# Optimization experiments

Measured on AMD Instinct MI355X. Metric: run time of the kernel, lower is better.

Reference implementation:

```python
import jax, jax.numpy as jnp
import numpy as np

N, E = 100000, 1600000
C_IN, C_HID, C_OUT = 64, 128, 64
EPS_MSG = 1e-7   # GENConv message eps
EPS_BN = 1e-5    # BatchNorm eps


def setup_inputs() -> dict:
    key = jax.random.key(0)
    ks = jax.random.split(key, 8)
    glorot = lambda k, shp, fan: jax.random.normal(k, shp, jnp.float32) * (1.0 / np.sqrt(fan))
    return dict(
        x=jax.random.normal(ks[0], (N, C_IN), jnp.float32),
        edge_index=jax.random.randint(ks[1], (2, E), 0, N, jnp.int32),
        edge_attr=jax.random.normal(ks[2], (E, C_IN), jnp.float32),
        pos=jax.random.normal(ks[3], (N, 3), jnp.float32),
        # GENConv internal MLP: Linear -> BN -> ReLU -> Linear
        W1=glorot(ks[4], (C_IN, C_HID), C_IN), b1=jnp.zeros((C_HID,), jnp.float32),
        g_mlp=jnp.ones((C_HID,), jnp.float32), be_mlp=jnp.zeros((C_HID,), jnp.float32),
        W2=glorot(ks[5], (C_HID, C_OUT), C_HID), b2=jnp.zeros((C_OUT,), jnp.float32),
        # block: BN -> SiLU -> Linear(no bias) -> BN -> SiLU
        g1=jnp.ones((C_OUT,), jnp.float32), be1=jnp.zeros((C_OUT,), jnp.float32),
        Wl=glorot(ks[6], (C_OUT, C_OUT), C_OUT),
        g2=jnp.ones((C_OUT,), jnp.float32), be2=jnp.zeros((C_OUT,), jnp.float32),
    )


def _bn(h, g, b):
    # training-mode batch norm over the node dimension
    m = h.mean(0)
    v = jnp.mean((h - m) ** 2, axis=0)
    return (h - m) * jax.lax.rsqrt(v + EPS_BN) * g + b


def reference(x, edge_index, edge_attr, pos, W1, b1, g_mlp, be_mlp, W2, b2,
              g1, be1, Wl, g2, be2):
    src, dst = edge_index[0], edge_index[1]
    # GENConv message: relu(x_j + e_attr) + eps, shape [E, C_IN]
    msg = jax.nn.relu(x[src] + edge_attr) + EPS_MSG
    # softmax aggregation over incoming edges per destination node (t = 1)
    mx = jax.ops.segment_max(msg, dst, num_segments=N)
    mx = jnp.where(jnp.isfinite(mx), mx, 0.0)  # guard empty segments
    ex = jnp.exp(msg - mx[dst])
    den = jax.ops.segment_sum(ex, dst, num_segments=N)
    w = ex / (den[dst] + 1e-16)
    aggr = jax.ops.segment_sum(msg * w, dst, num_segments=N)  # [N, C_IN]
    # root add + internal MLP (Linear -> BN -> ReLU -> Linear)
    h = aggr + x
    h = jax.nn.relu(_bn(h @ W1 + b1, g_mlp, be_mlp)) @ W2 + b2
    # block tail: BN -> SiLU -> Linear(no bias) -> BN -> SiLU
    h = jax.nn.silu(_bn(h, g1, be1))
    h = jax.nn.silu(_bn(h @ Wl, g2, be2))
    return h
```

## Files before the change

### kernel.cpp

```cpp
#include <hip/hip_runtime.h>

#define N_NODES 100000
#define E_EDGES 1600000
#define CIN 64
#define CHID 128
#define COUT 64
#define NT 64
#define NB ((N_NODES + NT - 1) / NT)
#define RBLK 64
#define CAP 128

__global__ void bucket_kernel(const int* __restrict__ ei, int* __restrict__ cnt,
                              int2* __restrict__ es) {
    int e = blockIdx.x * blockDim.x + threadIdx.x;
    if (e < E_EDGES) {
        int src = ei[e];
        int dst = ei[E_EDGES + e];
        int p = atomicAdd(&cnt[dst], 1);
        if (p < CAP) es[((long)dst << 7) + p] = make_int2(e, src);
    }
}

__global__ void gather_kernel(const float* __restrict__ x,
                              const float* __restrict__ ea,
                              const int2* __restrict__ es,
                              const int* __restrict__ cnt,
                              float* __restrict__ h0) {
    int node = (blockIdx.x * blockDim.x + threadIdx.x) >> 6;
    int lane = threadIdx.x & 63;
    if (node >= N_NODES) return;
    long s = (long)node << 7;
    int n = cnt[node];
    n = n > CAP ? CAP : n;
    float nm = 0.f, dn = 0.f;
    int p = 0;
    for (; p + 16 <= n; p += 16) {
        int2 q[16];
#pragma unroll
        for (int u = 0; u < 16; ++u) q[u] = es[s + p + u];
        float av[16], xv[16];
#pragma unroll
        for (int u = 0; u < 16; ++u)
            av[u] = __builtin_nontemporal_load(ea + (long)q[u].x * CIN + lane);
#pragma unroll
        for (int u = 0; u < 16; ++u) xv[u] = x[(long)q[u].y * CIN + lane];
#pragma unroll
        for (int u = 0; u < 16; ++u) {
            float m = fmaxf(xv[u] + av[u], 0.f) + 1e-7f;
            float ex = __expf(m);
            nm = fmaf(m, ex, nm);
            dn += ex;
        }
    }
    for (; p + 8 <= n; p += 8) {
        int2 q[8];
#pragma unroll
        for (int u = 0; u < 8; ++u) q[u] = es[s + p + u];
        float av[8], xv[8];
#pragma unroll
        for (int u = 0; u < 8; ++u)
            av[u] = __builtin_nontemporal_load(ea + (long)q[u].x * CIN + lane);
#pragma unroll
        for (int u = 0; u < 8; ++u) xv[u] = x[(long)q[u].y * CIN + lane];
#pragma unroll
        for (int u = 0; u < 8; ++u) {
            float m = fmaxf(xv[u] + av[u], 0.f) + 1e-7f;
            float ex = __expf(m);
            nm = fmaf(m, ex, nm);
            dn += ex;
        }
    }
    for (; p + 4 <= n; p += 4) {
        int2 q[4];
#pragma unroll
        for (int u = 0; u < 4; ++u) q[u] = es[s + p + u];
        float av[4], xv[4];
#pragma unroll
        for (int u = 0; u < 4; ++u)
            av[u] = __builtin_nontemporal_load(ea + (long)q[u].x * CIN + lane);
#pragma unroll
        for (int u = 0; u < 4; ++u) xv[u] = x[(long)q[u].y * CIN + lane];
#pragma unroll
        for (int u = 0; u < 4; ++u) {
            float m = fmaxf(xv[u] + av[u], 0.f) + 1e-7f;
            float ex = __expf(m);
            nm = fmaf(m, ex, nm);
            dn += ex;
        }
    }
    for (; p < n; ++p) {
        int2 q = es[s + p];
        float m = fmaxf(x[(long)q.y * CIN + lane] + ea[(long)q.x * CIN + lane], 0.f) + 1e-7f;
        float ex = __expf(m);
        nm = fmaf(m, ex, nm);
        dn += ex;
    }
    h0[(long)node * CIN + lane] = nm / (dn + 1e-16f) + x[(long)node * CIN + lane];
}

__global__ void reduce_slab_kernel(const float* __restrict__ P, int totrows,
                                   int rows_per, float* __restrict__ Q,
                                   float* __restrict__ mr, int C, float invN,
                                   int* __restrict__ ticket) {
    int C2 = blockDim.x;
    int t = threadIdx.x;
    long r0 = (long)blockIdx.x * rows_per;
    long r1 = r0 + rows_per;
    if (r1 > totrows) r1 = totrows;
    {
        float s0 = 0.f, s1 = 0.f, s2 = 0.f, s3 = 0.f;
        long r = r0;
        for (; r + 4 <= r1; r += 4) {
            s0 += P[(r + 0) * C2 + t];
            s1 += P[(r + 1) * C2 + t];
            s2 += P[(r + 2) * C2 + t];
            s3 += P[(r + 3) * C2 + t];
        }
        for (; r < r1; ++r) s0 += P[r * C2 + t];
        Q[(long)blockIdx.x * C2 + t] = (s0 + s1) + (s2 + s3);
    }
    __threadfence();
    __shared__ int lastFlag;
    if (t == 0) lastFlag = (atomicAdd(ticket, 1) == (int)gridDim.x - 1);
    __syncthreads();
    if (!lastFlag) return;
    __threadfence();
    float s0 = 0.f, s1 = 0.f, s2 = 0.f, s3 = 0.f;
    for (int r = 0; r < RBLK; r += 4) {
        s0 += Q[(long)(r + 0) * C2 + t];
        s1 += Q[(long)(r + 1) * C2 + t];
        s2 += Q[(long)(r + 2) * C2 + t];
        s3 += Q[(long)(r + 3) * C2 + t];
    }
    __shared__ float sm[256];
    sm[t] = (s0 + s1) + (s2 + s3);
    __syncthreads();
    if (t < C) {
        float m = sm[t] * invN;
        float v = sm[C + t] * invN - m * m;
        mr[t] = m;
        mr[C + t] = rsqrtf(fmaxf(v, 0.f) + 1e-5f);
    }
}

__global__ void __launch_bounds__(256) gemm1_kernel(
        const float* __restrict__ h0, const float* __restrict__ W1,
        const float* __restrict__ b1, float* __restrict__ t1,
        float* __restrict__ P) {
    __shared__ float sW[CIN * CHID];
    __shared__ float sh[NT * CIN];
    int tid = threadIdx.x;
    int nbase = blockIdx.x * NT;
    for (int i = tid * 4; i < CIN * CHID; i += 1024)
        *(float4*)&sW[i] = *(const float4*)&W1[i];
    for (int i = tid * 4; i < NT * CIN; i += 1024) {
        int node = nbase + (i >> 6);
        float4 v = make_float4(0.f, 0.f, 0.f, 0.f);
        if (node < N_NODES) v = *(const float4*)&h0[(long)node * CIN + (i & 63)];
        *(float4*)&sh[i] = v;
    }
    __syncthreads();
    int js = (tid & 31) * 4;
    int r  = tid >> 5;
    float4 bb = *(const float4*)&b1[js];
    float acc[8][4];
#pragma unroll
    for (int i = 0; i < 8; ++i) { acc[i][0]=bb.x; acc[i][1]=bb.y; acc[i][2]=bb.z; acc[i][3]=bb.w; }
#pragma unroll 4
    for (int k = 0; k < CIN; ++k) {
        float4 w = *(float4*)&sW[k * CHID + js];
#pragma unroll
        for (int i = 0; i < 8; ++i) {
            float a = sh[(r * 8 + i) * CIN + k];
            acc[i][0] = fmaf(a, w.x, acc[i][0]);
            acc[i][1] = fmaf(a, w.y, acc[i][1]);
            acc[i][2] = fmaf(a, w.z, acc[i][2]);
            acc[i][3] = fmaf(a, w.w, acc[i][3]);
        }
    }
    float s1[4] = {0,0,0,0}, s2[4] = {0,0,0,0};
#pragma unroll
    for (int i = 0; i < 8; ++i) {
        int node = nbase + r * 8 + i;
        if (node < N_NODES) {
            *(float4*)&t1[(long)node * CHID + js] =
                make_float4(acc[i][0], acc[i][1], acc[i][2], acc[i][3]);
#pragma unroll
            for (int jj = 0; jj < 4; ++jj) {
                s1[jj] += acc[i][jj];
                s2[jj] += acc[i][jj] * acc[i][jj];
            }
        }
    }
    __syncthreads();
    float* red = sW;
    *(float4*)&red[r * 128 + js]        = make_float4(s1[0], s1[1], s1[2], s1[3]);
    *(float4*)&red[1024 + r * 128 + js] = make_float4(s2[0], s2[1], s2[2], s2[3]);
    __syncthreads();
    {
        int base = (tid < 128) ? tid : (1024 + tid - 128);
        float v = 0.f;
#pragma unroll
        for (int rr = 0; rr < 8; ++rr) v += red[base + rr * 128];
        P[(long)blockIdx.x * 256 + tid] = v;
    }
}

__global__ void __launch_bounds__(256) gemm2_kernel(
        const float* __restrict__ t1, const float* __restrict__ mr1,
        const float* __restrict__ g, const float* __restrict__ be,
        const float* __restrict__ W2, const float* __restrict__ b2,
        float* __restrict__ h2, float* __restrict__ P) {
    __shared__ float sW[CHID * COUT];
    __shared__ float sr[NT * CHID];
    int tid = threadIdx.x;
    int nbase = blockIdx.x * NT;
    for (int i = tid * 4; i < CHID * COUT; i += 1024)
        *(float4*)&sW[i] = *(const float4*)&W2[i];
    for (int i = tid * 4; i < NT * CHID; i += 1024) {
        int node = nbase + (i >> 7);
        int j = i & 127;
        float4 v = make_float4(0.f, 0.f, 0.f, 0.f);
        if (node < N_NODES) {
            v = *(const float4*)&t1[(long)node * CHID + j];
            float4 mn = *(const float4*)&mr1[j];
            float4 rq = *(const float4*)&mr1[CHID + j];
            float4 gg = *(const float4*)&g[j];
            float4 bb = *(const float4*)&be[j];
            v.x = fmaxf((v.x - mn.x) * rq.x * gg.x + bb.x, 0.f);
            v.y = fmaxf((v.y - mn.y) * rq.y * gg.y + bb.y, 0.f);
            v.z = fmaxf((v.z - mn.z) * rq.z * gg.z + bb.z, 0.f);
            v.w = fmaxf((v.w - mn.w) * rq.w * gg.w + bb.w, 0.f);
        }
        *(float4*)&sr[i] = v;
    }
    __syncthreads();
    int js = (tid & 15) * 4;
    int r  = tid >> 4;
    float4 bb = *(const float4*)&b2[js];
    float acc[4][4];
#pragma unroll
    for (int i = 0; i < 4; ++i) { acc[i][0]=bb.x; acc[i][1]=bb.y; acc[i][2]=bb.z; acc[i][3]=bb.w; }
#pragma unroll 4
    for (int k = 0; k < CHID; ++k) {
        float4 w = *(float4*)&sW[k * COUT + js];
#pragma unroll
        for (int i = 0; i < 4; ++i) {
            float a = sr[(r * 4 + i) * CHID + k];
            acc[i][0] = fmaf(a, w.x, acc[i][0]);
            acc[i][1] = fmaf(a, w.y, acc[i][1]);
            acc[i][2] = fmaf(a, w.z, acc[i][2]);
            acc[i][3] = fmaf(a, w.w, acc[i][3]);
        }
    }
    float s1[4] = {0,0,0,0}, s2[4] = {0,0,0,0};
#pragma unroll
    for (int i = 0; i < 4; ++i) {
        int node = nbase + r * 4 + i;
        if (node < N_NODES) {
            *(float4*)&h2[(long)node * COUT + js] =
                make_float4(acc[i][0], acc[i][1], acc[i][2], acc[i][3]);
#pragma unroll
            for (int jj = 0; jj < 4; ++jj) {
                s1[jj] += acc[i][jj];
                s2[jj] += acc[i][jj] * acc[i][jj];
            }
        }
    }
    __syncthreads();
    float* red = sW;
    *(float4*)&red[r * 64 + js]        = make_float4(s1[0], s1[1], s1[2], s1[3]);
    *(float4*)&red[1024 + r * 64 + js] = make_float4(s2[0], s2[1], s2[2], s2[3]);
    __syncthreads();
    if (tid < 128) {
        int base = (tid < 64) ? tid : (1024 + tid - 64);
        float v = 0.f;
#pragma unroll
        for (int rr = 0; rr < 16; ++rr) v += red[base + rr * 64];
        P[(long)blockIdx.x * 128 + tid] = v;
    }
}

__global__ void __launch_bounds__(256) gemm3_kernel(
        const float* __restrict__ h2, const float* __restrict__ mr2,
        const float* __restrict__ g, const float* __restrict__ be,
        const float* __restrict__ Wl,
        float* __restrict__ t3, float* __restrict__ P) {
    __shared__ float sW[COUT * COUT];
    __shared__ float sr[NT * COUT];
    int tid = threadIdx.x;
    int nbase = blockIdx.x * NT;
    for (int i = tid * 4; i < COUT * COUT; i += 1024)
        *(float4*)&sW[i] = *(const float4*)&Wl[i];
    for (int i = tid * 4; i < NT * COUT; i += 1024) {
        int node = nbase + (i >> 6);
        int j = i & 63;
        float4 v = make_float4(0.f, 0.f, 0.f, 0.f);
        if (node < N_NODES) {
            v = *(const float4*)&h2[(long)node * COUT + j];
            float4 mn = *(const float4*)&mr2[j];
            float4 rq = *(const float4*)&mr2[COUT + j];
            float4 gg = *(const float4*)&g[j];
            float4 bb = *(const float4*)&be[j];
            v.x = (v.x - mn.x) * rq.x * gg.x + bb.x;
            v.y = (v.y - mn.y) * rq.y * gg.y + bb.y;
            v.z = (v.z - mn.z) * rq.z * gg.z + bb.z;
            v.w = (v.w - mn.w) * rq.w * gg.w + bb.w;
            v.x = v.x / (1.f + __expf(-v.x));
            v.y = v.y / (1.f + __expf(-v.y));
            v.z = v.z / (1.f + __expf(-v.z));
            v.w = v.w / (1.f + __expf(-v.w));
        }
        *(float4*)&sr[i] = v;
    }
    __syncthreads();
    int js = (tid & 15) * 4;
    int r  = tid >> 4;
    float acc[4][4];
#pragma unroll
    for (int i = 0; i < 4; ++i) { acc[i][0]=0.f; acc[i][1]=0.f; acc[i][2]=0.f; acc[i][3]=0.f; }
#pragma unroll 4
    for (int k = 0; k < COUT; ++k) {
        float4 w = *(float4*)&sW[k * COUT + js];
#pragma unroll
        for (int i = 0; i < 4; ++i) {
            float a = sr[(r * 4 + i) * COUT + k];
            acc[i][0] = fmaf(a, w.x, acc[i][0]);
            acc[i][1] = fmaf(a, w.y, acc[i][1]);
            acc[i][2] = fmaf(a, w.z, acc[i][2]);
            acc[i][3] = fmaf(a, w.w, acc[i][3]);
        }
    }
    float s1[4] = {0,0,0,0}, s2[4] = {0,0,0,0};
#pragma unroll
    for (int i = 0; i < 4; ++i) {
        int node = nbase + r * 4 + i;
        if (node < N_NODES) {
            *(float4*)&t3[(long)node * COUT + js] =
                make_float4(acc[i][0], acc[i][1], acc[i][2], acc[i][3]);
#pragma unroll
            for (int jj = 0; jj < 4; ++jj) {
                s1[jj] += acc[i][jj];
                s2[jj] += acc[i][jj] * acc[i][jj];
            }
        }
    }
    __syncthreads();
    float* red = sW;
    *(float4*)&red[r * 64 + js]        = make_float4(s1[0], s1[1], s1[2], s1[3]);
    *(float4*)&red[1024 + r * 64 + js] = make_float4(s2[0], s2[1], s2[2], s2[3]);
    __syncthreads();
    if (tid < 128) {
        int base = (tid < 64) ? tid : (1024 + tid - 64);
        float v = 0.f;
#pragma unroll
        for (int rr = 0; rr < 16; ++rr) v += red[base + rr * 64];
        P[(long)blockIdx.x * 128 + tid] = v;
    }
}

__global__ void final_kernel(const float* __restrict__ t3, const float* __restrict__ mr3,
                             const float* __restrict__ g, const float* __restrict__ be,
                             float* __restrict__ out) {
    long i = ((long)blockIdx.x * blockDim.x + threadIdx.x) * 4;
    int j = (int)(i & 63);
    float4 v = *(const float4*)&t3[i];
    float4 mn = *(const float4*)&mr3[j];
    float4 rq = *(const float4*)&mr3[COUT + j];
    float4 gg = *(const float4*)&g[j];
    float4 bb = *(const float4*)&be[j];
    v.x = (v.x - mn.x) * rq.x * gg.x + bb.x;
    v.y = (v.y - mn.y) * rq.y * gg.y + bb.y;
    v.z = (v.z - mn.z) * rq.z * gg.z + bb.z;
    v.w = (v.w - mn.w) * rq.w * gg.w + bb.w;
    v.x = v.x / (1.f + __expf(-v.x));
    v.y = v.y / (1.f + __expf(-v.y));
    v.z = v.z / (1.f + __expf(-v.z));
    v.w = v.w / (1.f + __expf(-v.w));
    *(float4*)&out[i] = v;
}

extern "C" void kernel_launch(void* const* d_in, const int* in_sizes, int n_in,
                              void* d_out, int out_size, void* d_ws, size_t ws_size,
                              hipStream_t stream) {
    const float* x   = (const float*)d_in[0];
    const int*   ei  = (const int*)d_in[1];
    const float* ea  = (const float*)d_in[2];
    const float* W1  = (const float*)d_in[4];
    const float* b1  = (const float*)d_in[5];
    const float* gm  = (const float*)d_in[6];
    const float* bm  = (const float*)d_in[7];
    const float* W2  = (const float*)d_in[8];
    const float* b2  = (const float*)d_in[9];
    const float* g1  = (const float*)d_in[10];
    const float* be1 = (const float*)d_in[11];
    const float* Wl  = (const float*)d_in[12];
    const float* g2  = (const float*)d_in[13];
    const float* be2 = (const float*)d_in[14];
    float* out = (float*)d_out;

    float* h0   = (float*)d_ws;
    float* t1   = h0 + (long)N_NODES * CIN;
    float* h2   = t1 + (long)N_NODES * CHID;
    float* t3   = h0;
    float* Sfin = h2 + (long)N_NODES * COUT;
    float* Q    = Sfin + 512;
    int*   cnt  = (int*)(Q + RBLK * 256);
    int*   tickets = cnt + N_NODES;
    long   es_off = ((long)(N_NODES * CIN) + (long)N_NODES * CHID + (long)N_NODES * COUT
                     + 512 + RBLK * 256 + N_NODES + 4 + 255) & ~255L;
    int2*  es   = (int2*)((float*)d_ws + es_off);
    float* P1 = h2;
    float* P2 = h0;
    float* P3 = t1;

    const float invN = 1.f / N_NODES;

    hipMemsetAsync(cnt, 0, ((size_t)N_NODES + 4) * sizeof(int), stream);

    bucket_kernel<<<(E_EDGES + 255) / 256, 256, 0, stream>>>(ei, cnt, es);
    gather_kernel<<<(N_NODES * 64 + 255) / 256, 256, 0, stream>>>(x, ea, es, cnt, h0);

    const int rpA = (NB + RBLK - 1) / RBLK;

    gemm1_kernel<<<NB, 256, 0, stream>>>(h0, W1, b1, t1, P1);
    reduce_slab_kernel<<<RBLK, 256, 0, stream>>>(P1, NB, rpA, Q, Sfin, CHID, invN, tickets + 0);
    gemm2_kernel<<<NB, 256, 0, stream>>>(t1, Sfin, gm, bm, W2, b2, h2, P2);
    reduce_slab_kernel<<<RBLK, 128, 0, stream>>>(P2, NB, rpA, Q, Sfin + 256, COUT, invN, tickets + 1);
    gemm3_kernel<<<NB, 256, 0, stream>>>(h2, Sfin + 256, g1, be1, Wl, t3, P3);
    reduce_slab_kernel<<<RBLK, 128, 0, stream>>>(P3, NB, rpA, Q, Sfin + 384, COUT, invN, tickets + 2);
    final_kernel<<<(N_NODES * COUT / 4) / 256, 256, 0, stream>>>(t3, Sfin + 384, g2, be2, out);
}
```

Measured before the change: 371.7 us.

## Compute first BN stats from input second moments and fuse GEMM1 with GEMM2

The first batch-norm statistics are now derived algebraically from the mean and 64x64 second-moment matrix of h0 combined with W1, so the 128-wide hidden activation no longer has to be written out first. GEMM1 and GEMM2 are fused into one kernel that keeps the hidden tile in LDS, which removes the t1 write and re-read and one launch. Bias b1 is dropped because the batch norm cancels it. The trade-offs are an extra moment pass over h0, 80KB of LDS per block (which lowers occupancy), and possible cancellation error in the E[x²]-mean² variance formula.

Result: slower. 449.7 us (+21.0%).

```diff
diff --git a/kernel.cpp b/kernel.cpp
--- a/kernel.cpp
+++ b/kernel.cpp
@@ -9,6 +9,9 @@
 #define NB ((N_NODES + NT - 1) / NT)
 #define RBLK 64
 #define CAP 128
+#define SBLK 256
+#define SROWS ((N_NODES + SBLK - 1) / SBLK)
+#define SPSTRIDE 4160
 
 __global__ void bucket_kernel(const int* __restrict__ ei, int* __restrict__ cnt,
                               int2* __restrict__ es) {
@@ -96,6 +99,197 @@
         dn += ex;
     }
     h0[(long)node * CIN + lane] = nm / (dn + 1e-16f) + x[(long)node * CIN + lane];
+}
+
+__global__ void __launch_bounds__(256) smom_kernel(const float* __restrict__ h0,
+                                                   float* __restrict__ Sp) {
+    __shared__ float sh[64 * 64];
+    int tid = threadIdx.x;
+    int i4 = (tid & 15) * 4;
+    int j4 = (tid >> 4) * 4;
+    float acc[4][4];
+#pragma unroll
+    for (int a = 0; a < 4; ++a) { acc[a][0]=0.f; acc[a][1]=0.f; acc[a][2]=0.f; acc[a][3]=0.f; }
+    float msum = 0.f;
+    int n0 = blockIdx.x * SROWS;
+    int n1 = n0 + SROWS;
+    if (n1 > N_NODES) n1 = N_NODES;
+    for (int t0 = n0; t0 < n1; t0 += 64) {
+        int tn = n1 - t0; if (tn > 64) tn = 64;
+        __syncthreads();
+        for (int idx = tid * 4; idx < 64 * 64; idx += 1024) {
+            int nl = idx >> 6;
+            float4 v = make_float4(0.f, 0.f, 0.f, 0.f);
+            if (nl < tn) v = *(const float4*)&h0[(long)(t0 + nl) * CIN + (idx & 63)];
+            *(float4*)&sh[idx] = v;
+        }
+        __syncthreads();
+#pragma unroll 2
+        for (int nl = 0; nl < tn; ++nl) {
+            float hi[4], hj[4];
+#pragma unroll
+            for (int a = 0; a < 4; ++a) hi[a] = sh[nl * 64 + i4 + a];
+#pragma unroll
+            for (int b = 0; b < 4; ++b) hj[b] = sh[nl * 64 + j4 + b];
+#pragma unroll
+            for (int a = 0; a < 4; ++a)
+#pragma unroll
+                for (int b = 0; b < 4; ++b) acc[a][b] = fmaf(hi[a], hj[b], acc[a][b]);
+            if (tid < 64) msum += sh[nl * 64 + tid];
+        }
+    }
+    float* p = Sp + (long)blockIdx.x * SPSTRIDE;
+#pragma unroll
+    for (int a = 0; a < 4; ++a)
+        *(float4*)&p[(i4 + a) * 64 + j4] = make_float4(acc[a][0], acc[a][1], acc[a][2], acc[a][3]);
+    if (tid < 64) p[4096 + tid] = msum;
+}
+
+__global__ void __launch_bounds__(256) sred_kernel(const float* __restrict__ Sp,
+        const float* __restrict__ W1, float* __restrict__ Sfull,
+        float* __restrict__ mr1, float invN, int* __restrict__ ticket) {
+    int tid = threadIdx.x;
+    int idx = blockIdx.x * 256 + tid;
+    float s = 0.f;
+    for (int p = 0; p < SBLK; ++p) s += Sp[(long)p * SPSTRIDE + idx];
+    Sfull[idx] = s;
+    if (blockIdx.x == 0 && tid < 64) {
+        float m = 0.f;
+        for (int p = 0; p < SBLK; ++p) m += Sp[(long)p * SPSTRIDE + 4096 + tid];
+        Sfull[4096 + tid] = m;
+    }
+    __threadfence();
+    __shared__ int lastFlag;
+    if (tid == 0) lastFlag = (atomicAdd(ticket, 1) == (int)gridDim.x - 1);
+    __syncthreads();
+    if (!lastFlag) return;
+    __threadfence();
+    __shared__ float sS[4096 + 64];
+    __shared__ float sW[CIN * CHID];
+    __shared__ float redQ[256], redM[256];
+    for (int k = tid; k < 4096 + 64; k += 256) sS[k] = Sfull[k];
+    for (int k = tid; k < CIN * CHID; k += 256) sW[k] = W1[k];
+    __syncthreads();
+    int j = tid & 127;
+    int half = tid >> 7;
+    float q = 0.f, ml = 0.f;
+    for (int i = half * 32; i < half * 32 + 32; ++i) {
+        float wi = sW[i * CHID + j];
+        float inner = 0.f;
+#pragma unroll 4
+        for (int k = 0; k < 64; ++k) inner = fmaf(sS[i * 64 + k], sW[k * CHID + j], inner);
+        q = fmaf(wi, inner, q);
+        ml = fmaf(sS[4096 + i], wi, ml);
+    }
+    redQ[tid] = q; redM[tid] = ml;
+    __syncthreads();
+    if (tid < 128) {
+        float qf = redQ[tid] + redQ[tid + 128];
+        float mlf = (redM[tid] + redM[tid + 128]) * invN;
+        float var = qf * invN - mlf * mlf;
+        mr1[tid] = mlf;
+        mr1[128 + tid] = rsqrtf(fmaxf(var, 0.f) + 1e-5f);
+    }
+}
+
+__global__ void __launch_bounds__(256) gemm12_kernel(
+        const float* __restrict__ h0, const float* __restrict__ W1,
+        const float* __restrict__ mr1, const float* __restrict__ g1v,
+        const float* __restrict__ be1v,
+        const float* __restrict__ W2, const float* __restrict__ b2,
+        float* __restrict__ h2, float* __restrict__ P) {
+    __shared__ float lds[20480];
+    float* sW1 = lds;
+    float* sW2 = lds + 8192;
+    float* sh  = lds + 16384;
+    int tid = threadIdx.x;
+    int nbase = blockIdx.x * NT;
+    for (int i = tid * 4; i < 8192; i += 1024) *(float4*)&sW1[i] = *(const float4*)&W1[i];
+    for (int i = tid * 4; i < 8192; i += 1024) *(float4*)&sW2[i] = *(const float4*)&W2[i];
+    for (int i = tid * 4; i < 4096; i += 1024) {
+        int node = nbase + (i >> 6);
+        float4 v = make_float4(0.f, 0.f, 0.f, 0.f);
+        if (node < N_NODES) v = *(const float4*)&h0[(long)node * CIN + (i & 63)];
+        *(float4*)&sh[i] = v;
+    }
+    __syncthreads();
+    int js = (tid & 31) * 4;
+    int r  = tid >> 5;
+    float acc[8][4];
+#pragma unroll
+    for (int i = 0; i < 8; ++i) { acc[i][0]=0.f; acc[i][1]=0.f; acc[i][2]=0.f; acc[i][3]=0.f; }
+#pragma unroll 4
+    for (int k = 0; k < CIN; ++k) {
+        float4 w = *(float4*)&sW1[k * CHID + js];
+#pragma unroll
+        for (int i = 0; i < 8; ++i) {
+            float a = sh[(r * 8 + i) * CIN + k];
+            acc[i][0] = fmaf(a, w.x, acc[i][0]);
+            acc[i][1] = fmaf(a, w.y, acc[i][1]);
+            acc[i][2] = fmaf(a, w.z, acc[i][2]);
+            acc[i][3] = fmaf(a, w.w, acc[i][3]);
+        }
+    }
+    float4 mn = *(const float4*)&mr1[js];
+    float4 rs = *(const float4*)&mr1[128 + js];
+    float4 gg = *(const float4*)&g1v[js];
+    float4 bb = *(const float4*)&be1v[js];
+    __syncthreads();
+    float* sr = lds;
+#pragma unroll
+    for (int i = 0; i < 8; ++i) {
+        float4 v;
+        v.x = fmaxf((acc[i][0] - mn.x) * rs.x * gg.x + bb.x, 0.f);
+        v.y = fmaxf((acc[i][1] - mn.y) * rs.y * gg.y + bb.y, 0.f);
+        v.z = fmaxf((acc[i][2] - mn.z) * rs.z * gg.z + bb.z, 0.f);
+        v.w = fmaxf((acc[i][3] - mn.w) * rs.w * gg.w + bb.w, 0.f);
+        *(float4*)&sr[(r * 8 + i) * CHID + js] = v;
+    }
+    __syncthreads();
+    int js2 = (tid & 15) * 4;
+    int r2  = tid >> 4;
+    float4 b2v = *(const float4*)&b2[js2];
+    float acc2[4][4];
+#pragma unroll
+    for (int i = 0; i < 4; ++i) { acc2[i][0]=b2v.x; acc2[i][1]=b2v.y; acc2[i][2]=b2v.z; acc2[i][3]=b2v.w; }
+#pragma unroll 4
+    for (int k = 0; k < CHID; ++k) {
+        float4 w = *(float4*)&sW2[k * COUT + js2];
+#pragma unroll
+        for (int i = 0; i < 4; ++i) {
+            float a = sr[(r2 * 4 + i) * CHID + k];
+            acc2[i][0] = fmaf(a, w.x, acc2[i][0]);
+            acc2[i][1] = fmaf(a, w.y, acc2[i][1]);
+            acc2[i][2] = fmaf(a, w.z, acc2[i][2]);
+            acc2[i][3] = fmaf(a, w.w, acc2[i][3]);
+        }
+    }
+    float s1[4] = {0,0,0,0}, s2[4] = {0,0,0,0};
+#pragma unroll
+    for (int i = 0; i < 4; ++i) {
+        int node = nbase + r2 * 4 + i;
+        if (node < N_NODES) {
+            *(float4*)&h2[(long)node * COUT + js2] =
+                make_float4(acc2[i][0], acc2[i][1], acc2[i][2], acc2[i][3]);
+#pragma unroll
+            for (int jj = 0; jj < 4; ++jj) {
+                s1[jj] += acc2[i][jj];
+                s2[jj] += acc2[i][jj] * acc2[i][jj];
+            }
+        }
+    }
+    __syncthreads();
+    float* red = lds + 16384;
+    *(float4*)&red[r2 * 64 + js2]        = make_float4(s1[0], s1[1], s1[2], s1[3]);
+    *(float4*)&red[1024 + r2 * 64 + js2] = make_float4(s2[0], s2[1], s2[2], s2[3]);
+    __syncthreads();
+    if (tid < 128) {
+        int base = (tid < 64) ? tid : (1024 + tid - 64);
+        float v = 0.f;
+#pragma unroll
+        for (int rr = 0; rr < 16; ++rr) v += red[base + rr * 64];
+        P[(long)blockIdx.x * 128 + tid] = v;
+    }
 }
 
 __global__ void reduce_slab_kernel(const float* __restrict__ P, int totrows,
@@ -140,144 +334,6 @@
         float v = sm[C + t] * invN - m * m;
         mr[t] = m;
         mr[C + t] = rsqrtf(fmaxf(v, 0.f) + 1e-5f);
-    }
-}
-
-__global__ void __launch_bounds__(256) gemm1_kernel(
-        const float* __restrict__ h0, const float* __restrict__ W1,
-        const float* __restrict__ b1, float* __restrict__ t1,
-        float* __restrict__ P) {
-    __shared__ float sW[CIN * CHID];
-    __shared__ float sh[NT * CIN];
-    int tid = threadIdx.x;
-    int nbase = blockIdx.x * NT;
-    for (int i = tid * 4; i < CIN * CHID; i += 1024)
-        *(float4*)&sW[i] = *(const float4*)&W1[i];
-    for (int i = tid * 4; i < NT * CIN; i += 1024) {
-        int node = nbase + (i >> 6);
-        float4 v = make_float4(0.f, 0.f, 0.f, 0.f);
-        if (node < N_NODES) v = *(const float4*)&h0[(long)node * CIN + (i & 63)];
-        *(float4*)&sh[i] = v;
-    }
-    __syncthreads();
-    int js = (tid & 31) * 4;
-    int r  = tid >> 5;
-    float4 bb = *(const float4*)&b1[js];
-    float acc[8][4];
-#pragma unroll
-    for (int i = 0; i < 8; ++i) { acc[i][0]=bb.x; acc[i][1]=bb.y; acc[i][2]=bb.z; acc[i][3]=bb.w; }
-#pragma unroll 4
-    for (int k = 0; k < CIN; ++k) {
-        float4 w = *(float4*)&sW[k * CHID + js];
-#pragma unroll
-        for (int i = 0; i < 8; ++i) {
-            float a = sh[(r * 8 + i) * CIN + k];
-            acc[i][0] = fmaf(a, w.x, acc[i][0]);
-            acc[i][1] = fmaf(a, w.y, acc[i][1]);
-            acc[i][2] = fmaf(a, w.z, acc[i][2]);
-            acc[i][3] = fmaf(a, w.w, acc[i][3]);
-        }
-    }
-    float s1[4] = {0,0,0,0}, s2[4] = {0,0,0,0};
-#pragma unroll
-    for (int i = 0; i < 8; ++i) {
-        int node = nbase + r * 8 + i;
-        if (node < N_NODES) {
-            *(float4*)&t1[(long)node * CHID + js] =
-                make_float4(acc[i][0], acc[i][1], acc[i][2], acc[i][3]);
-#pragma unroll
-            for (int jj = 0; jj < 4; ++jj) {
-                s1[jj] += acc[i][jj];
-                s2[jj] += acc[i][jj] * acc[i][jj];
-            }
-        }
-    }
-    __syncthreads();
-    float* red = sW;
-    *(float4*)&red[r * 128 + js]        = make_float4(s1[0], s1[1], s1[2], s1[3]);
-    *(float4*)&red[1024 + r * 128 + js] = make_float4(s2[0], s2[1], s2[2], s2[3]);
-    __syncthreads();
-    {
-        int base = (tid < 128) ? tid : (1024 + tid - 128);
-        float v = 0.f;
-#pragma unroll
-        for (int rr = 0; rr < 8; ++rr) v += red[base + rr * 128];
-        P[(long)blockIdx.x * 256 + tid] = v;
-    }
-}
-
-__global__ void __launch_bounds__(256) gemm2_kernel(
-        const float* __restrict__ t1, const float* __restrict__ mr1,
-        const float* __restrict__ g, const float* __restrict__ be,
-        const float* __restrict__ W2, const float* __restrict__ b2,
-        float* __restrict__ h2, float* __restrict__ P) {
-    __shared__ float sW[CHID * COUT];
-    __shared__ float sr[NT * CHID];
-    int tid = threadIdx.x;
-    int nbase = blockIdx.x * NT;
-    for (int i = tid * 4; i < CHID * COUT; i += 1024)
-        *(float4*)&sW[i] = *(const float4*)&W2[i];
-    for (int i = tid * 4; i < NT * CHID; i += 1024) {
-        int node = nbase + (i >> 7);
-        int j = i & 127;
-        float4 v = make_float4(0.f, 0.f, 0.f, 0.f);
-        if (node < N_NODES) {
-            v = *(const float4*)&t1[(long)node * CHID + j];
-            float4 mn = *(const float4*)&mr1[j];
-            float4 rq = *(const float4*)&mr1[CHID + j];
-            float4 gg = *(const float4*)&g[j];
-            float4 bb = *(const float4*)&be[j];
-            v.x = fmaxf((v.x - mn.x) * rq.x * gg.x + bb.x, 0.f);
-            v.y = fmaxf((v.y - mn.y) * rq.y * gg.y + bb.y, 0.f);
-            v.z = fmaxf((v.z - mn.z) * rq.z * gg.z + bb.z, 0.f);
-            v.w = fmaxf((v.w - mn.w) * rq.w * gg.w + bb.w, 0.f);
-        }
-        *(float4*)&sr[i] = v;
-    }
-    __syncthreads();
-    int js = (tid & 15) * 4;
-    int r  = tid >> 4;
-    float4 bb = *(const float4*)&b2[js];
-    float acc[4][4];
-#pragma unroll
-    for (int i = 0; i < 4; ++i) { acc[i][0]=bb.x; acc[i][1]=bb.y; acc[i][2]=bb.z; acc[i][3]=bb.w; }
-#pragma unroll 4
-    for (int k = 0; k < CHID; ++k) {
-        float4 w = *(float4*)&sW[k * COUT + js];
-#pragma unroll
-        for (int i = 0; i < 4; ++i) {
-            float a = sr[(r * 4 + i) * CHID + k];
-            acc[i][0] = fmaf(a, w.x, acc[i][0]);
-            acc[i][1] = fmaf(a, w.y, acc[i][1]);
-            acc[i][2] = fmaf(a, w.z, acc[i][2]);
-            acc[i][3] = fmaf(a, w.w, acc[i][3]);
-        }
-    }
-    float s1[4] = {0,0,0,0}, s2[4] = {0,0,0,0};
-#pragma unroll
-    for (int i = 0; i < 4; ++i) {
-        int node = nbase + r * 4 + i;
-        if (node < N_NODES) {
-            *(float4*)&h2[(long)node * COUT + js] =
-                make_float4(acc[i][0], acc[i][1], acc[i][2], acc[i][3]);
-#pragma unroll
-            for (int jj = 0; jj < 4; ++jj) {
-                s1[jj] += acc[i][jj];
-                s2[jj] += acc[i][jj] * acc[i][jj];
-            }
-        }
-    }
-    __syncthreads();
-    float* red = sW;
-    *(float4*)&red[r * 64 + js]        = make_float4(s1[0], s1[1], s1[2], s1[3]);
-    *(float4*)&red[1024 + r * 64 + js] = make_float4(s2[0], s2[1], s2[2], s2[3]);
-    __syncthreads();
-    if (tid < 128) {
-        int base = (tid < 64) ? tid : (1024 + tid - 64);
-        float v = 0.f;
-#pragma unroll
-        for (int rr = 0; rr < 16; ++rr) v += red[base + rr * 64];
-        P[(long)blockIdx.x * 128 + tid] = v;
     }
 }
 
@@ -387,7 +443,6 @@
     const int*   ei  = (const int*)d_in[1];
     const float* ea  = (const float*)d_in[2];
     const float* W1  = (const float*)d_in[4];
-    const float* b1  = (const float*)d_in[5];
     const float* gm  = (const float*)d_in[6];
     const float* bm  = (const float*)d_in[7];
     const float* W2  = (const float*)d_in[8];
@@ -400,8 +455,8 @@
     float* out = (float*)d_out;
 
     float* h0   = (float*)d_ws;
-    float* t1   = h0 + (long)N_NODES * CIN;
-    float* h2   = t1 + (long)N_NODES * CHID;
+    float* scr  = h0 + (long)N_NODES * CIN;
+    float* h2   = scr + (long)N_NODES * CHID;
     float* t3   = h0;
     float* Sfin = h2 + (long)N_NODES * COUT;
     float* Q    = Sfin + 512;
@@ -410,9 +465,10 @@
     long   es_off = ((long)(N_NODES * CIN) + (long)N_NODES * CHID + (long)N_NODES * COUT
                      + 512 + RBLK * 256 + N_NODES + 4 + 255) & ~255L;
     int2*  es   = (int2*)((float*)d_ws + es_off);
-    float* P1 = h2;
-    float* P2 = h0;
-    float* P3 = t1;
+    float* Sp    = scr;
+    float* Sfull = scr + 1100000;
+    float* P2    = scr + 1200000;
+    float* P3    = scr + 1500000;
 
     const float invN = 1.f / N_NODES;
 
@@ -421,11 +477,12 @@
     bucket_kernel<<<(E_EDGES + 255) / 256, 256, 0, stream>>>(ei, cnt, es);
     gather_kernel<<<(N_NODES * 64 + 255) / 256, 256, 0, stream>>>(x, ea, es, cnt, h0);
 
+    smom_kernel<<<SBLK, 256, 0, stream>>>(h0, Sp);
+    sred_kernel<<<16, 256, 0, stream>>>(Sp, W1, Sfull, Sfin, invN, tickets + 0);
+
     const int rpA = (NB + RBLK - 1) / RBLK;
 
-    gemm1_kernel<<<NB, 256, 0, stream>>>(h0, W1, b1, t1, P1);
-    reduce_slab_kernel<<<RBLK, 256, 0, stream>>>(P1, NB, rpA, Q, Sfin, CHID, invN, tickets + 0);
-    gemm2_kernel<<<NB, 256, 0, stream>>>(t1, Sfin, gm, bm, W2, b2, h2, P2);
+    gemm12_kernel<<<NB, 256, 0, stream>>>(h0, W1, Sfin, gm, bm, W2, b2, h2, P2);
     reduce_slab_kernel<<<RBLK, 128, 0, stream>>>(P2, NB, rpA, Q, Sfin + 256, COUT, invN, tickets + 1);
     gemm3_kernel<<<NB, 256, 0, stream>>>(h2, Sfin + 256, g1, be1, Wl, t3, P3);
     reduce_slab_kernel<<<RBLK, 128, 0, stream>>>(P3, NB, rpA, Q, Sfin + 384, COUT, invN, tickets + 2);
```
